# Kernel optimization log

Hardware: AMD Instinct MI355X
Metric: run time of the kernel (lower is better)

The kernel has to match this reference:

```python
import jax, jax.numpy as jnp
import numpy as np
from jax import lax

WIN = 7            # win_size
K = 0.03           # stability constant
COV_NORM = WIN * WIN / (WIN * WIN - 1.0)  # faithful: win_size**2 / (win_size**2 - 1)


def setup_inputs() -> dict:
    key = jax.random.key(0)
    kx, ky = jax.random.split(key)
    x = jax.random.normal(kx, (2, 4, 160, 160, 96), dtype=jnp.float32)
    y = jax.random.randint(ky, (2, 1, 160, 160, 96), 0, 4, dtype=jnp.int64)
    return {"x": x, "y": y}


def _box_mean(a):
    s = lax.reduce_window(a, jnp.array(0, a.dtype), lax.add,
                          (1, 1, WIN, WIN, WIN), (1, 1, 1, 1, 1), 'VALID')
    return s / jnp.asarray(WIN ** 3, a.dtype)


def reference(x, y):
    B, C, H, W, D = x.shape
    # one_hot(y, num_classes=C): (B,1,H,W,D) int -> (B,C,H,W,D) float
    y1 = jnp.moveaxis(jax.nn.one_hot(y[:, 0], C, dtype=x.dtype), -1, 1)
    xr = x.reshape(-1, 1, H, W, D)
    yr = y1.reshape(-1, 1, H, W, D)
    xr = xr * yr
    data_range = jnp.max(yr)
    xr = jax.nn.sigmoid(xr)
    c = (K * data_range) ** 2 / 2
    ux = _box_mean(xr)
    uy = _box_mean(yr)
    uxx = _box_mean(xr * xr)
    uyy = _box_mean(yr * yr)
    uxy = _box_mean(xr * yr)
    vx = COV_NORM * (uxx - ux * ux)
    vy = COV_NORM * (uyy - uy * uy)
    vxy = COV_NORM * (uxy - ux * uy)
    s_value = (vxy + c) / (vx * vy + c)
    return 1.0 - jnp.mean(s_value)
```

## Files before the change

### kernel.cpp

```cpp
#include <hip/hip_runtime.h>
#include <hip/hip_fp16.h>

#define WINS 7
#define H 160
#define W 160
#define DD 96
#define HO 154
#define WO 154
#define DOUT 90
#define CSTRIDE (H*W*DD)

#define TH 8
#define TW 8
#define TD 16
#define IH 14
#define IW 14
#define NCOL (IH * IW)
#define IDU 22
#define NDP 11
#define ID 24
#define NV 6
#define NITEMS (NCOL * NV)
#define HTILES 20
#define WTILES 20
#define DTILES 6
#define DPB2 24

struct alignas(8) Half4 { __half x, y, z, w; };

static __device__ __forceinline__ __half2 u2h(unsigned int a) {
    __half2 r; __builtin_memcpy(&r, &a, 4); return r;
}
static __device__ __forceinline__ unsigned int h2u(__half2 v) {
    unsigned int r; __builtin_memcpy(&r, &v, 4); return r;
}
static __device__ __forceinline__ void pmask(__half2 v, __half2& p, __half2& m) {
    const unsigned int bits = h2u(v);
    const unsigned int neg  = bits & 0x80008000u;
    const unsigned int full = (neg >> 15) * 0xFFFFu;
    p = u2h(bits & ~full);
    m = u2h(((~bits >> 15) & 0x00010001u) * 0x3C00u);
}

__device__ __forceinline__ float sval(float c0, float c1, float c2) {
    const float S_t  = c1 + 0.5f  * (343.0f - c0);
    const float S_t2 = c2 + 0.25f * (343.0f - c0);
    const float inv  = 1.0f / 343.0f;
    const float ux   = S_t  * inv;
    const float uy   = c0   * inv;
    const float uxx  = S_t2 * inv;
    const float uxy  = c1   * inv;
    const float covn = 49.0f / 48.0f;
    const float cc   = 0.00045f;
    const float vx  = covn * (uxx - ux * ux);
    const float vy  = covn * (uy  - uy * uy);
    const float vxy = covn * (uxy - ux * uy);
    return (vxy + cc) * __builtin_amdgcn_rcpf(vx * vy + cc);
}

__global__ __launch_bounds__(256, 5)
void structure_loss_main(const float* __restrict__ x,
                         const int* __restrict__ y,
                         double* __restrict__ acc) {
    __shared__ __half sA0[IH * TW * IDU];
    __shared__ __half sA1[IH * TW * IDU];
    __shared__ __half sA2[IH * TW * IDU];
    __shared__ union alignas(16) {
        __half vs[NCOL * ID];
        struct {
            __half b0[TH * TW * DPB2];
            __half b1[TH * TW * DPB2];
            __half b2[TH * TW * DPB2];
        } sb;
    } u;
    __shared__ unsigned int yb[NCOL * 2];
    __shared__ float wsum[4];

    const int dt = blockIdx.x;
    const int wt = blockIdx.y;
    const int z  = blockIdx.z;
    const int b  = z / HTILES;
    const int ht = z - b * HTILES;

    const int h0 = ht * TH, w0 = wt * TW, d0 = dt * TD;
    const int* yc = y + (size_t)b * (size_t)CSTRIDE;
    const int t = threadIdx.x;

    for (int i = t; i < NCOL * 2; i += 256) {
        const int col = i >> 1, hf = i & 1;
        const int ih = col / IW, iw = col - ih * IW;
        const int h = min(h0 + ih, H - 1);
        const int w = min(w0 + iw, W - 1);
        const size_t cb = (size_t)(h * W + w) * DD;
        const int dstart = d0 + 12 * hf;
        unsigned int pk = 0u;
#pragma unroll
        for (int j3 = 0; j3 < 3; j3++) {
            const int dbase = dstart + 4 * j3;
            if (dbase < DD) {
                const int4 yv = *(const int4*)(yc + cb + dbase);
                pk |= (unsigned)(yv.x & 3) << (2 * (4 * j3 + 0));
                pk |= (unsigned)(yv.y & 3) << (2 * (4 * j3 + 1));
                pk |= (unsigned)(yv.z & 3) << (2 * (4 * j3 + 2));
                pk |= (unsigned)(yv.w & 3) << (2 * (4 * j3 + 3));
            }
        }
        yb[i] = pk;
    }
    __syncthreads();

    float lsum = 0.f;

    for (int cl = 0; cl < 4; cl++) {
        const float* xc = x + ((size_t)b * 4 + cl) * (size_t)CSTRIDE;

#pragma unroll
        for (int k = 0; k < 5; k++) {
            const int i = t + 256 * k;
            if (i < NITEMS) {
                const int col = i / NV, q = i - col * NV;
                const int ih = col / IW, iw = col - ih * IW;
                const int h = min(h0 + ih, H - 1);
                const int w = min(w0 + iw, W - 1);
                const int dbase = d0 + 4 * q;
                Half4 hv;
                hv.x = hv.y = hv.z = hv.w = __float2half(0.f);
                if (dbase < DD) {
                    const float4 xv = *(const float4*)(xc + (h * W + w) * DD + dbase);
                    const int wsel = (q >= 3) ? 1 : 0;
                    const unsigned int pk =
                        yb[col * 2 + wsel] >> (8 * (q - 3 * wsel));
                    const float s0 = 1.0f / (1.0f + __expf(-xv.x));
                    const float s1 = 1.0f / (1.0f + __expf(-xv.y));
                    const float s2 = 1.0f / (1.0f + __expf(-xv.z));
                    const float s3 = 1.0f / (1.0f + __expf(-xv.w));
                    hv.x = __float2half(((int)((pk >> 0) & 3u) == cl) ? s0 : -s0);
                    hv.y = __float2half(((int)((pk >> 2) & 3u) == cl) ? s1 : -s1);
                    hv.z = __float2half(((int)((pk >> 4) & 3u) == cl) ? s2 : -s2);
                    hv.w = __float2half(((int)((pk >> 6) & 3u) == cl) ? s3 : -s3);
                }
                *(Half4*)&u.vs[col * ID + 4 * q] = hv;
            }
        }
        __syncthreads();

        if (t < IH * NDP) {
            const int ih = t / NDP, dp = t - ih * NDP;
            const int dd = 2 * dp;
            const __half2 z2 = __float2half2_rn(0.f);
            __half2 v2[IW];
            const int vbase = ih * IW * ID + dd;
#pragma unroll
            for (int iw = 0; iw < IW; iw++)
                v2[iw] = *(const __half2*)&u.vs[vbase + iw * ID];
            __half2 sm = z2, sp = z2, sq = z2;
#pragma unroll
            for (int iw = 0; iw < WINS; iw++) {
                __half2 p, m;
                pmask(v2[iw], p, m);
                sm = __hadd2(sm, m);
                sp = __hadd2(sp, p);
                sq = __hfma2(p, v2[iw], sq);
            }
            int o = (ih * TW) * IDU + dd;
            *(__half2*)&sA0[o] = sm;
            *(__half2*)&sA1[o] = sp;
            *(__half2*)&sA2[o] = sq;
#pragma unroll
            for (int wo = 1; wo < TW; wo++) {
                const __half2 a = v2[wo + 6], bb = v2[wo - 1];
                __half2 pa, ma, pb, mb;
                pmask(a, pa, ma);
                pmask(bb, pb, mb);
                sm = __hadd2(sm, __hsub2(ma, mb));
                sp = __hadd2(sp, __hsub2(pa, pb));
                sq = __hadd2(sq, __hsub2(__hmul2(pa, a), __hmul2(pb, bb)));
                o += IDU;
                *(__half2*)&sA0[o] = sm;
                *(__half2*)&sA1[o] = sp;
                *(__half2*)&sA2[o] = sq;
            }
        }
        __syncthreads();

        if (t < 2 * TW * NDP) {
            const int dp = t % NDP;
            const int r  = t / NDP;
            const int wo = r & 7;
            const int ho0 = (r >> 3) * 4;
            const int dd = 2 * dp;
            __half2 a0[10], a1[10], a2[10];
#pragma unroll
            for (int k = 0; k < 10; k++) {
                const int idx = ((ho0 + k) * TW + wo) * IDU + dd;
                a0[k] = *(const __half2*)&sA0[idx];
                a1[k] = *(const __half2*)&sA1[idx];
                a2[k] = *(const __half2*)&sA2[idx];
            }
            __half2 s0 = a0[0], s1 = a1[0], s2 = a2[0];
#pragma unroll
            for (int k = 1; k < WINS; k++) {
                s0 = __hadd2(s0, a0[k]);
                s1 = __hadd2(s1, a1[k]);
                s2 = __hadd2(s2, a2[k]);
            }
            int o = (ho0 * TW + wo) * DPB2 + dd;
            *(__half2*)&u.sb.b0[o] = s0;
            *(__half2*)&u.sb.b1[o] = s1;
            *(__half2*)&u.sb.b2[o] = s2;
#pragma unroll
            for (int k = 1; k < 4; k++) {
                s0 = __hadd2(s0, __hsub2(a0[k + 6], a0[k - 1]));
                s1 = __hadd2(s1, __hsub2(a1[k + 6], a1[k - 1]));
                s2 = __hadd2(s2, __hsub2(a2[k + 6], a2[k - 1]));
                o += TW * DPB2;
                *(__half2*)&u.sb.b0[o] = s0;
                *(__half2*)&u.sb.b1[o] = s1;
                *(__half2*)&u.sb.b2[o] = s2;
            }
        }
        __syncthreads();

        {
            const int dq = t & 3;
            const int wo = (t >> 2) & 7;
            const int ho = t >> 5;
            const int hg = h0 + ho, wg = w0 + wo;
            if (hg < HO && wg < WO) {
                const int base = (ho * TW + wo) * DPB2 + dq * 4;
                float b0[10], b1[10], b2[10];
#pragma unroll
                for (int k = 0; k < 5; k++) {
                    float2 f;
                    f = __half22float2(*(const __half2*)&u.sb.b0[base + 2 * k]);
                    b0[2 * k] = f.x; b0[2 * k + 1] = f.y;
                    f = __half22float2(*(const __half2*)&u.sb.b1[base + 2 * k]);
                    b1[2 * k] = f.x; b1[2 * k + 1] = f.y;
                    f = __half22float2(*(const __half2*)&u.sb.b2[base + 2 * k]);
                    b2[2 * k] = f.x; b2[2 * k + 1] = f.y;
                }
                float s0 = 0.f, s1 = 0.f, s2 = 0.f;
#pragma unroll
                for (int k = 0; k < WINS; k++) { s0 += b0[k]; s1 += b1[k]; s2 += b2[k]; }
                const int dg = d0 + dq * 4;
#pragma unroll
                for (int k = 0; k < 4; k++) {
                    if (k > 0) {
                        s0 += b0[k + 6] - b0[k - 1];
                        s1 += b1[k + 6] - b1[k - 1];
                        s2 += b2[k + 6] - b2[k - 1];
                    }
                    if (dg + k < DOUT) lsum += sval(s0, s1, s2);
                }
            }
        }
        __syncthreads();
    }

#pragma unroll
    for (int off = 32; off > 0; off >>= 1) lsum += __shfl_down(lsum, off, 64);
    const int wave = t >> 6;
    if ((t & 63) == 0) wsum[wave] = lsum;
    __syncthreads();
    if (t == 0) {
        const float s = wsum[0] + wsum[1] + wsum[2] + wsum[3];
        atomicAdd(acc, (double)s);
    }
}

__global__ void structure_loss_finalize(const double* __restrict__ acc,
                                        float* __restrict__ out) {
    out[0] = 1.0f - (float)(acc[0] / 17075520.0);
}

extern "C" void kernel_launch(void* const* d_in, const int* in_sizes, int n_in,
                              void* d_out, int out_size, void* d_ws, size_t ws_size,
                              hipStream_t stream) {
    const float* x = (const float*)d_in[0];
    const int*   y = (const int*)d_in[1];
    double* acc = (double*)d_ws;

    (void)hipMemsetAsync(d_ws, 0, sizeof(double), stream);

    dim3 grid(DTILES, WTILES, 2 * HTILES);
    structure_loss_main<<<grid, 256, 0, stream>>>(x, y, acc);
    structure_loss_finalize<<<1, 1, 0, stream>>>(acc, (float*)d_out);
}
```

Measured before the change: 221.0 us.

## Precompute signed sigmoid in fp16 via prepass kernel to cut halo re-reads

After: 211.9 us. 4.1% less time.

```diff
diff --git a/kernel.cpp b/kernel.cpp
--- a/kernel.cpp
+++ b/kernel.cpp
@@ -58,9 +58,36 @@
     return (vxy + cc) * __builtin_amdgcn_rcpf(vx * vy + cc);
 }
 
+__global__ __launch_bounds__(256)
+void sigmoid_prepass(const float* __restrict__ x,
+                     const int* __restrict__ y,
+                     __half* __restrict__ xs) {
+    const int b  = blockIdx.y;
+    const int qv = blockIdx.x * 256 + threadIdx.x;
+    const int off = 4 * qv;
+    const int4 yv = *(const int4*)(y + (size_t)b * CSTRIDE + off);
+#pragma unroll
+    for (int c = 0; c < 4; c++) {
+        const size_t xo = ((size_t)(b * 4 + c)) * CSTRIDE + off;
+        const float4 xv = *(const float4*)(x + xo);
+        const float s0 = 1.0f / (1.0f + __expf(-xv.x));
+        const float s1 = 1.0f / (1.0f + __expf(-xv.y));
+        const float s2 = 1.0f / (1.0f + __expf(-xv.z));
+        const float s3 = 1.0f / (1.0f + __expf(-xv.w));
+        Half4 hv;
+        hv.x = __float2half((yv.x == c) ? s0 : -s0);
+        hv.y = __float2half((yv.y == c) ? s1 : -s1);
+        hv.z = __float2half((yv.z == c) ? s2 : -s2);
+        hv.w = __float2half((yv.w == c) ? s3 : -s3);
+        *(Half4*)(xs + xo) = hv;
+    }
+}
+
+template <bool PRE>
 __global__ __launch_bounds__(256, 5)
 void structure_loss_main(const float* __restrict__ x,
                          const int* __restrict__ y,
+                         const __half* __restrict__ xs,
                          double* __restrict__ acc) {
     __shared__ __half sA0[IH * TW * IDU];
     __shared__ __half sA1[IH * TW * IDU];
@@ -86,60 +113,80 @@
     const int* yc = y + (size_t)b * (size_t)CSTRIDE;
     const int t = threadIdx.x;
 
-    for (int i = t; i < NCOL * 2; i += 256) {
-        const int col = i >> 1, hf = i & 1;
-        const int ih = col / IW, iw = col - ih * IW;
-        const int h = min(h0 + ih, H - 1);
-        const int w = min(w0 + iw, W - 1);
-        const size_t cb = (size_t)(h * W + w) * DD;
-        const int dstart = d0 + 12 * hf;
-        unsigned int pk = 0u;
-#pragma unroll
-        for (int j3 = 0; j3 < 3; j3++) {
-            const int dbase = dstart + 4 * j3;
-            if (dbase < DD) {
-                const int4 yv = *(const int4*)(yc + cb + dbase);
-                pk |= (unsigned)(yv.x & 3) << (2 * (4 * j3 + 0));
-                pk |= (unsigned)(yv.y & 3) << (2 * (4 * j3 + 1));
-                pk |= (unsigned)(yv.z & 3) << (2 * (4 * j3 + 2));
-                pk |= (unsigned)(yv.w & 3) << (2 * (4 * j3 + 3));
-            }
-        }
-        yb[i] = pk;
-    }
-    __syncthreads();
+    if (!PRE) {
+        for (int i = t; i < NCOL * 2; i += 256) {
+            const int col = i >> 1, hf = i & 1;
+            const int ih = col / IW, iw = col - ih * IW;
+            const int h = min(h0 + ih, H - 1);
+            const int w = min(w0 + iw, W - 1);
+            const size_t cb = (size_t)(h * W + w) * DD;
+            const int dstart = d0 + 12 * hf;
+            unsigned int pk = 0u;
+#pragma unroll
+            for (int j3 = 0; j3 < 3; j3++) {
+                const int dbase = dstart + 4 * j3;
+                if (dbase < DD) {
+                    const int4 yv = *(const int4*)(yc + cb + dbase);
+                    pk |= (unsigned)(yv.x & 3) << (2 * (4 * j3 + 0));
+                    pk |= (unsigned)(yv.y & 3) << (2 * (4 * j3 + 1));
+                    pk |= (unsigned)(yv.z & 3) << (2 * (4 * j3 + 2));
+                    pk |= (unsigned)(yv.w & 3) << (2 * (4 * j3 + 3));
+                }
+            }
+            yb[i] = pk;
+        }
+        __syncthreads();
+    }
 
     float lsum = 0.f;
 
     for (int cl = 0; cl < 4; cl++) {
-        const float* xc = x + ((size_t)b * 4 + cl) * (size_t)CSTRIDE;
-
-#pragma unroll
-        for (int k = 0; k < 5; k++) {
-            const int i = t + 256 * k;
-            if (i < NITEMS) {
-                const int col = i / NV, q = i - col * NV;
-                const int ih = col / IW, iw = col - ih * IW;
-                const int h = min(h0 + ih, H - 1);
-                const int w = min(w0 + iw, W - 1);
-                const int dbase = d0 + 4 * q;
-                Half4 hv;
-                hv.x = hv.y = hv.z = hv.w = __float2half(0.f);
-                if (dbase < DD) {
-                    const float4 xv = *(const float4*)(xc + (h * W + w) * DD + dbase);
-                    const int wsel = (q >= 3) ? 1 : 0;
-                    const unsigned int pk =
-                        yb[col * 2 + wsel] >> (8 * (q - 3 * wsel));
-                    const float s0 = 1.0f / (1.0f + __expf(-xv.x));
-                    const float s1 = 1.0f / (1.0f + __expf(-xv.y));
-                    const float s2 = 1.0f / (1.0f + __expf(-xv.z));
-                    const float s3 = 1.0f / (1.0f + __expf(-xv.w));
-                    hv.x = __float2half(((int)((pk >> 0) & 3u) == cl) ? s0 : -s0);
-                    hv.y = __float2half(((int)((pk >> 2) & 3u) == cl) ? s1 : -s1);
-                    hv.z = __float2half(((int)((pk >> 4) & 3u) == cl) ? s2 : -s2);
-                    hv.w = __float2half(((int)((pk >> 6) & 3u) == cl) ? s3 : -s3);
-                }
-                *(Half4*)&u.vs[col * ID + 4 * q] = hv;
+        if (PRE) {
+            const __half* xsc = xs + ((size_t)b * 4 + cl) * (size_t)CSTRIDE;
+#pragma unroll
+            for (int k = 0; k < 3; k++) {
+                const int i = t + 256 * k;
+                if (i < NCOL * 3) {
+                    const int col = i / 3, q = i - col * 3;
+                    const int ih = col / IW, iw = col - ih * IW;
+                    const int h = min(h0 + ih, H - 1);
+                    const int w = min(w0 + iw, W - 1);
+                    const int dbase = d0 + 8 * q;
+                    uint4 vv = make_uint4(0u, 0u, 0u, 0u);
+                    if (dbase < DD)
+                        vv = *(const uint4*)(xsc + (h * W + w) * DD + dbase);
+                    *(uint4*)&u.vs[col * ID + 8 * q] = vv;
+                }
+            }
+        } else {
+            const float* xc = x + ((size_t)b * 4 + cl) * (size_t)CSTRIDE;
+#pragma unroll
+            for (int k = 0; k < 5; k++) {
+                const int i = t + 256 * k;
+                if (i < NITEMS) {
+                    const int col = i / NV, q = i - col * NV;
+                    const int ih = col / IW, iw = col - ih * IW;
+                    const int h = min(h0 + ih, H - 1);
+                    const int w = min(w0 + iw, W - 1);
+                    const int dbase = d0 + 4 * q;
+                    Half4 hv;
+                    hv.x = hv.y = hv.z = hv.w = __float2half(0.f);
+                    if (dbase < DD) {
+                        const float4 xv = *(const float4*)(xc + (h * W + w) * DD + dbase);
+                        const int wsel = (q >= 3) ? 1 : 0;
+                        const unsigned int pk =
+                            yb[col * 2 + wsel] >> (8 * (q - 3 * wsel));
+                        const float s0 = 1.0f / (1.0f + __expf(-xv.x));
+                        const float s1 = 1.0f / (1.0f + __expf(-xv.y));
+                        const float s2 = 1.0f / (1.0f + __expf(-xv.z));
+                        const float s3 = 1.0f / (1.0f + __expf(-xv.w));
+                        hv.x = __float2half(((int)((pk >> 0) & 3u) == cl) ? s0 : -s0);
+                        hv.y = __float2half(((int)((pk >> 2) & 3u) == cl) ? s1 : -s1);
+                        hv.z = __float2half(((int)((pk >> 4) & 3u) == cl) ? s2 : -s2);
+                        hv.w = __float2half(((int)((pk >> 6) & 3u) == cl) ? s3 : -s3);
+                    }
+                    *(Half4*)&u.vs[col * ID + 4 * q] = hv;
+                }
             }
         }
         __syncthreads();
@@ -279,10 +326,18 @@
     const float* x = (const float*)d_in[0];
     const int*   y = (const int*)d_in[1];
     double* acc = (double*)d_ws;
+    __half* xs = (__half*)((char*)d_ws + 16);
 
     (void)hipMemsetAsync(d_ws, 0, sizeof(double), stream);
 
+    const size_t need = 16 + (size_t)8 * CSTRIDE * sizeof(__half);
     dim3 grid(DTILES, WTILES, 2 * HTILES);
-    structure_loss_main<<<grid, 256, 0, stream>>>(x, y, acc);
+
+    if (ws_size >= need) {
+        sigmoid_prepass<<<dim3(2400, 2), 256, 0, stream>>>(x, y, xs);
+        structure_loss_main<true><<<grid, 256, 0, stream>>>(x, y, xs, acc);
+    } else {
+        structure_loss_main<false><<<grid, 256, 0, stream>>>(x, y, xs, acc);
+    }
     structure_loss_finalize<<<1, 1, 0, stream>>>(acc, (float*)d_out);
 }
```
